# Kernel tuning notes

Hardware: AMD Instinct MI355X
Metric: run time of the kernel (lower is better)

## Reference

```python
import jax, jax.numpy as jnp
import numpy as np

B, C, Q, D = 64, 512, 64, 256  # D = 2 * hidden_size; similarity weight has 3*D = 768 entries


def _length_mask(key, batch, seqlen):
    # realistic padding masks: each row has a random valid prefix length in [seqlen//2, seqlen]
    lens = jax.random.randint(key, (batch,), seqlen // 2, seqlen + 1)
    return (jnp.arange(seqlen)[None, :] < lens[:, None]).astype(jnp.int32)


def setup_inputs() -> dict:
    key = jax.random.key(0)
    k1, k2, k3, k4, k5 = jax.random.split(key, 5)
    context = jax.random.normal(k1, (B, C, D), dtype=jnp.float32)
    question = jax.random.normal(k2, (B, Q, D), dtype=jnp.float32)
    context_mask = _length_mask(k3, B, C)
    question_mask = _length_mask(k4, B, Q)
    w = jax.random.normal(k5, (3 * D,), dtype=jnp.float32) * (1.0 / np.sqrt(3 * D))
    return {"context": context, "question": question,
            "context_mask": context_mask, "question_mask": question_mask, "w": w}


def reference(context, question, context_mask, question_mask, w):
    d = context.shape[-1]
    # Linear([c, q, c*q]) with no bias decomposes exactly into three terms.
    w_c, w_q, w_m = w[:d], w[d:2 * d], w[2 * d:]
    sim = ((context @ w_c)[:, :, None]                      # [B, C, 1]
           + (question @ w_q)[:, None, :]                   # [B, 1, Q]
           + jnp.einsum('bcd,bqd->bcq', context * w_m, question))  # [B, C, Q]
    neg = jnp.finfo(sim.dtype).min
    # context-to-query attention (mask question positions)
    sim_q = jnp.where(question_mask[:, None, :] != 0, sim, neg)
    a = jax.nn.softmax(sim_q, axis=2)                        # [B, C, Q]
    c2q = jnp.einsum('bcq,bqd->bcd', a, question)            # [B, C, D]
    # query-to-context attention (max over Q, mask context positions)
    sim_max = jnp.max(sim, axis=2)                           # [B, C]
    sim_max = jnp.where(context_mask != 0, sim_max, neg)
    b = jax.nn.softmax(sim_max, axis=1)                      # [B, C]
    q2c = jnp.einsum('bc,bcd->bd', b, context)[:, None, :]   # [B, 1, D]
    q2c = jnp.broadcast_to(q2c, context.shape)               # [B, C, D]
    g = jnp.concatenate([context, c2q, context * c2q, context * q2c], axis=-1)
    return g
```

## Files before the change

kernel.cpp:

```cpp
#include <hip/hip_runtime.h>
#include <hip/hip_bf16.h>
#include <float.h>

#define B_ 64
#define C_ 512
#define Q_ 64
#define D_ 256

typedef _Float16 f16x8 __attribute__((ext_vector_type(8)));
typedef float f32x4 __attribute__((ext_vector_type(4)));

union U4H8 { uint4 u; f16x8 h; };
union UH2 { _Float16 h[2]; uint32_t u; };

__device__ __forceinline__ uint32_t packh2(float a, float b) {
  UH2 v; v.h[0] = (_Float16)a; v.h[1] = (_Float16)b; return v.u;
}

__device__ __forceinline__ float wred_sum(float v) {
#pragma unroll
  for (int off = 32; off > 0; off >>= 1) v += __shfl_xor(v, off, 64);
  return v;
}
__device__ __forceinline__ float wred_max(float v) {
#pragma unroll
  for (int off = 32; off > 0; off >>= 1) v = fmaxf(v, __shfl_xor(v, off, 64));
  return v;
}

__global__ __launch_bounds__(256) void k_rowdot(const float* __restrict__ src,
                                                const float* __restrict__ wgt,
                                                float* __restrict__ out, int nrows) {
  int wv = threadIdx.x >> 6, ln = threadIdx.x & 63;
  int row = blockIdx.x * 4 + wv;
  if (row >= nrows) return;
  float4 s4 = *(const float4*)(src + (size_t)row * D_ + 4 * ln);
  float4 w4 = *(const float4*)(wgt + 4 * ln);
  float p = s4.x * w4.x + s4.y * w4.y + s4.z * w4.z + s4.w * w4.w;
  p = wred_sum(p);
  if (ln == 0) out[row] = p;
}

__global__ __launch_bounds__(256) void k_prepack(const float* __restrict__ qst,
                                                 const float* __restrict__ w,
                                                 uint32_t* __restrict__ qraw_img,
                                                 uint32_t* __restrict__ qT_img,
                                                 float* __restrict__ qwq) {
  const int b = blockIdx.x;
  const int sub = blockIdx.y;
  const int t = threadIdx.x;
  const float* qb = qst + (size_t)b * Q_ * D_;
#pragma unroll
  for (int it = 0; it < 8; ++it) {
    int idx = sub * 2048 + it * 256 + t;
    int q = idx >> 7, jp = idx & 127;
    float2 v = *(const float2*)(qb + q * D_ + 2 * jp);
    int ch = jp >> 2;
    int phys = (ch & ~7) | ((ch & 7) ^ (q & 7));
    qraw_img[(size_t)b * 8192 + q * 128 + phys * 4 + (jp & 3)] = packh2(v.x, v.y);
  }
  {
    int d = sub * 64 + (t >> 2);
    uint32_t* dst = qT_img + (size_t)b * 8192 + d * 32;
#pragma unroll
    for (int k = 0; k < 2; ++k) {
      int qc = (t & 3) * 2 + k;
      uint32_t tmp[4];
#pragma unroll
      for (int e = 0; e < 4; ++e) {
        int q0 = qc * 8 + e * 2;
        tmp[e] = packh2(qb[q0 * D_ + d], qb[(q0 + 1) * D_ + d]);
      }
      int pc = qc ^ (d & 7);
      *(uint4*)(dst + pc * 4) = uint4{tmp[0], tmp[1], tmp[2], tmp[3]};
    }
  }
  if (sub == 0) {
    int q = t >> 2, sl = t & 3;
    float p = 0.f;
#pragma unroll
    for (int i = 0; i < 16; ++i) {
      float4 v = *(const float4*)(qb + q * D_ + sl * 64 + i * 4);
      float4 ww = *(const float4*)(w + D_ + sl * 64 + i * 4);
      p += v.x * ww.x + v.y * ww.y + v.z * ww.z + v.w * ww.w;
    }
    p += __shfl_xor(p, 1, 64);
    p += __shfl_xor(p, 2, 64);
    if (sl == 0) qwq[b * Q_ + q] = p;
  }
}

__global__ __launch_bounds__(256, 4) void k_sim(
    const float* __restrict__ ctx, const int* __restrict__ qmask,
    const float* __restrict__ w, const float* __restrict__ qwq_g,
    const uint32_t* __restrict__ qraw_img,
    ushort* __restrict__ P_img, float* __restrict__ simmax_g) {
  __shared__ __align__(16) ushort qraw[Q_ * D_];
  __shared__ float qwq_l[Q_];
  __shared__ int   qml_l[Q_];

  const int bid = blockIdx.x;
  const int b = bid & 63;
  const int c0 = (bid >> 6) * 64;
  const int t = threadIdx.x;
  const int wv = t >> 6, ln = t & 63;
  const int lc = ln & 15;
  const int lg = ln >> 4;
  const int c0w = c0 + wv * 16;

  {
    const uint32_t* qr_src = qraw_img + (size_t)b * 8192;
#pragma unroll
    for (int i = 0; i < 8; ++i)
      __builtin_amdgcn_global_load_lds(
          (const __attribute__((address_space(1))) uint32_t*)(qr_src + i * 1024 + t * 4),
          (__attribute__((address_space(3))) uint32_t*)((uint32_t*)qraw + i * 1024 + t * 4),
          16, 0, 0);
  }

  f16x8 bfrag[8];
  float cwc_p = 0.f;
  const float* crow = ctx + ((size_t)b * C_ + c0w + lc) * D_;
#pragma unroll
  for (int kk = 0; kk < 8; ++kk) {
    int kb = kk * 32 + lg * 8;
    float4 cv0 = *(const float4*)(crow + kb);
    float4 cv1 = *(const float4*)(crow + kb + 4);
    float4 wc0 = *(const float4*)(w + kb);
    float4 wc1 = *(const float4*)(w + kb + 4);
    float4 wm0 = *(const float4*)(w + 2 * D_ + kb);
    float4 wm1 = *(const float4*)(w + 2 * D_ + kb + 4);
    cwc_p += cv0.x * wc0.x + cv0.y * wc0.y + cv0.z * wc0.z + cv0.w * wc0.w
           + cv1.x * wc1.x + cv1.y * wc1.y + cv1.z * wc1.z + cv1.w * wc1.w;
    bfrag[kk][0] = (_Float16)(cv0.x * wm0.x);
    bfrag[kk][1] = (_Float16)(cv0.y * wm0.y);
    bfrag[kk][2] = (_Float16)(cv0.z * wm0.z);
    bfrag[kk][3] = (_Float16)(cv0.w * wm0.w);
    bfrag[kk][4] = (_Float16)(cv1.x * wm1.x);
    bfrag[kk][5] = (_Float16)(cv1.y * wm1.y);
    bfrag[kk][6] = (_Float16)(cv1.z * wm1.z);
    bfrag[kk][7] = (_Float16)(cv1.w * wm1.w);
  }
  float cwc = cwc_p;
  cwc += __shfl_xor(cwc, 16, 64);
  cwc += __shfl_xor(cwc, 32, 64);

  if (t < Q_) { qwq_l[t] = qwq_g[b * Q_ + t]; qml_l[t] = qmask[b * Q_ + t]; }
  __syncthreads();

  f32x4 sacc[4];
#pragma unroll
  for (int tq = 0; tq < 4; ++tq) sacc[tq] = f32x4{0.f, 0.f, 0.f, 0.f};
#pragma unroll
  for (int tq = 0; tq < 4; ++tq) {
    int q = 16 * tq + lc;
#pragma unroll
    for (int kk = 0; kk < 8; ++kk) {
      int ch = lg + 4 * kk;
      int phys = (ch & ~7) | ((ch & 7) ^ (q & 7));
      U4H8 a; a.u = *(const uint4*)((const char*)qraw + q * 512 + phys * 16);
      sacc[tq] = __builtin_amdgcn_mfma_f32_16x16x32_f16(a.h, bfrag[kk], sacc[tq], 0, 0, 0);
    }
  }

  float vals[4][4];
  float rmax = -FLT_MAX;
#pragma unroll
  for (int tq = 0; tq < 4; ++tq) {
    float4 qw4 = *(const float4*)(qwq_l + 16 * tq + 4 * lg);
#pragma unroll
    for (int r = 0; r < 4; ++r) {
      float qv = (r == 0) ? qw4.x : (r == 1) ? qw4.y : (r == 2) ? qw4.z : qw4.w;
      vals[tq][r] = sacc[tq][r] + cwc + qv;
      rmax = fmaxf(rmax, vals[tq][r]);
    }
  }
  rmax = fmaxf(rmax, __shfl_xor(rmax, 16, 64));
  rmax = fmaxf(rmax, __shfl_xor(rmax, 32, 64));
  if (ln < 16) simmax_g[b * C_ + c0w + lc] = rmax;

  float mmax = -FLT_MAX;
#pragma unroll
  for (int tq = 0; tq < 4; ++tq) {
    int4 qm4 = *(const int4*)(qml_l + 16 * tq + 4 * lg);
#pragma unroll
    for (int r = 0; r < 4; ++r) {
      int m = (r == 0) ? qm4.x : (r == 1) ? qm4.y : (r == 2) ? qm4.z : qm4.w;
      vals[tq][r] = m ? vals[tq][r] : -FLT_MAX;
      mmax = fmaxf(mmax, vals[tq][r]);
    }
  }
  mmax = fmaxf(mmax, __shfl_xor(mmax, 16, 64));
  mmax = fmaxf(mmax, __shfl_xor(mmax, 32, 64));
  float esum = 0.f;
#pragma unroll
  for (int tq = 0; tq < 4; ++tq)
#pragma unroll
    for (int r = 0; r < 4; ++r) {
      vals[tq][r] = __expf(vals[tq][r] - mmax);
      esum += vals[tq][r];
    }
  esum += __shfl_xor(esum, 16, 64);
  esum += __shfl_xor(esum, 32, 64);
  float inv = 1.f / esum;
  char* pdst = (char*)(P_img + ((size_t)bid * 4 + wv) * 1024);
#pragma unroll
  for (int tq = 0; tq < 4; ++tq) {
    uint32_t p01 = packh2(vals[tq][0] * inv, vals[tq][1] * inv);
    uint32_t p23 = packh2(vals[tq][2] * inv, vals[tq][3] * inv);
    int qb4 = 16 * tq + 4 * lg;
    *(uint2*)(pdst + lc * 128 + qb4 * 2) = uint2{p01, p23};
  }
}

__global__ __launch_bounds__(256, 4) void k_c2q(
    const float* __restrict__ ctx, const uint32_t* __restrict__ qT_img,
    const ushort* __restrict__ P_img, const float* __restrict__ part,
    float* __restrict__ g) {
  __shared__ __align__(16) ushort qT[D_ * Q_];
  __shared__ float q2c_l[D_];

  const int bid = blockIdx.x;
  const int b = bid & 63;
  const int c0 = (bid >> 6) * 64;
  const int t = threadIdx.x;
  const int wv = t >> 6, ln = t & 63;
  const int lc = ln & 15;
  const int lg = ln >> 4;
  const int c0w = c0 + wv * 16;

  {
    const uint32_t* qt_src = qT_img + (size_t)b * 8192;
#pragma unroll
    for (int i = 0; i < 8; ++i)
      __builtin_amdgcn_global_load_lds(
          (const __attribute__((address_space(1))) uint32_t*)(qt_src + i * 1024 + t * 4),
          (__attribute__((address_space(3))) uint32_t*)((uint32_t*)qT + i * 1024 + t * 4),
          16, 0, 0);
  }
  const char* psrc = (const char*)(P_img + ((size_t)bid * 4 + wv) * 1024);
  U4H8 pf0, pf1;
  pf0.u = *(const uint4*)(psrc + lc * 128 + lg * 16);
  pf1.u = *(const uint4*)(psrc + lc * 128 + lg * 16 + 64);
  {
    float s = 0.f;
#pragma unroll
    for (int k = 0; k < 8; ++k) s += part[((size_t)b * 8 + k) * D_ + t];
    q2c_l[t] = s;
  }
  __syncthreads();

  const float* crow2 = ctx + ((size_t)b * C_ + c0w + lc) * D_;
  float* grow = g + ((size_t)b * C_ + c0w + lc) * (4 * D_);
#pragma unroll 4
  for (int dt = 0; dt < 16; ++dt) {
    f32x4 acc = f32x4{0.f, 0.f, 0.f, 0.f};
    {
      int d = dt * 16 + lc;
      int phys0 = lg ^ (d & 7);
      int phys1 = (lg + 4) ^ (d & 7);
      U4H8 aq0; aq0.u = *(const uint4*)((const char*)qT + d * 128 + phys0 * 16);
      U4H8 aq1; aq1.u = *(const uint4*)((const char*)qT + d * 128 + phys1 * 16);
      acc = __builtin_amdgcn_mfma_f32_16x16x32_f16(aq0.h, pf0.h, acc, 0, 0, 0);
      acc = __builtin_amdgcn_mfma_f32_16x16x32_f16(aq1.h, pf1.h, acc, 0, 0, 0);
    }
    int dcol = dt * 16 + 4 * lg;
    float4 cvv = *(const float4*)(crow2 + dcol);
    float4 q4 = *(const float4*)(q2c_l + dcol);
    *(float4*)(grow + dcol) = cvv;
    float4 c2qv{acc[0], acc[1], acc[2], acc[3]};
    *(float4*)(grow + D_ + dcol) = c2qv;
    float4 p2{cvv.x * c2qv.x, cvv.y * c2qv.y, cvv.z * c2qv.z, cvv.w * c2qv.w};
    *(float4*)(grow + 2 * D_ + dcol) = p2;
    float4 p3{cvv.x * q4.x, cvv.y * q4.y, cvv.z * q4.z, cvv.w * q4.w};
    *(float4*)(grow + 3 * D_ + dcol) = p3;
  }
}

__global__ __launch_bounds__(256) void k_q2c_bs(const float* __restrict__ ctx,
                                                const float* __restrict__ simmax,
                                                const int* __restrict__ cmask,
                                                float* __restrict__ part) {
  int b = blockIdx.x, ch = blockIdx.y, t = threadIdx.x;
  int wv = t >> 6, ln = t & 63;
  __shared__ float bls[C_];
  __shared__ float sred[4];
  __shared__ float ssum[4];
  float v0 = simmax[b * C_ + t], v1 = simmax[b * C_ + 256 + t];
  if (!cmask[b * C_ + t]) v0 = -FLT_MAX;
  if (!cmask[b * C_ + 256 + t]) v1 = -FLT_MAX;
  float mx = wred_max(fmaxf(v0, v1));
  if (ln == 0) sred[wv] = mx;
  __syncthreads();
  float bm = fmaxf(fmaxf(sred[0], sred[1]), fmaxf(sred[2], sred[3]));
  float e0 = __expf(v0 - bm), e1 = __expf(v1 - bm);
  float ps = wred_sum(e0 + e1);
  if (ln == 0) ssum[wv] = ps;
  __syncthreads();
  float bs = ssum[0] + ssum[1] + ssum[2] + ssum[3];
  float invbs = 1.f / bs;
  bls[t] = e0 * invbs;
  bls[256 + t] = e1 * invbs;
  __syncthreads();
  float acc = 0.f;
  int cbeg = ch * 64;
#pragma unroll 4
  for (int c = cbeg; c < cbeg + 64; ++c)
    acc += bls[c] * ctx[((size_t)b * C_ + c) * D_ + t];
  part[((size_t)b * 8 + ch) * D_ + t] = acc;
}

__global__ __launch_bounds__(256, 2) void k_main_fb(
    const float* __restrict__ ctx, const float* __restrict__ qst,
    const int* __restrict__ qmask, const float* __restrict__ w,
    const float* __restrict__ qwq_g, float* __restrict__ g,
    float* __restrict__ simmax_g) {
  __shared__ __align__(16) ushort qraw[Q_ * D_];
  __shared__ __align__(16) ushort qT[D_ * Q_];
  __shared__ __align__(16) ushort pbuf[4][16 * Q_];
  __shared__ float qwq_l[Q_];
  __shared__ int   qml_l[Q_];

  const int bid = blockIdx.x;
  const int b = bid & 63;
  const int c0 = (bid >> 6) * 64;
  const int t = threadIdx.x;
  const int wv = t >> 6, ln = t & 63;
  const int lc = ln & 15;
  const int lg = ln >> 4;
  const int c0w = c0 + wv * 16;
  const float* qb = qst + (size_t)b * Q_ * D_;

  f16x8 bfrag[8];
  float cwc_p = 0.f;
  const float* crow = ctx + ((size_t)b * C_ + c0w + lc) * D_;
  float* grow0 = g + ((size_t)b * C_ + c0w + lc) * (4 * D_);
#pragma unroll
  for (int kk = 0; kk < 8; ++kk) {
    int kb = kk * 32 + lg * 8;
    float4 cv0 = *(const float4*)(crow + kb);
    float4 cv1 = *(const float4*)(crow + kb + 4);
    float4 wc0 = *(const float4*)(w + kb);
    float4 wc1 = *(const float4*)(w + kb + 4);
    float4 wm0 = *(const float4*)(w + 2 * D_ + kb);
    float4 wm1 = *(const float4*)(w + 2 * D_ + kb + 4);
    cwc_p += cv0.x * wc0.x + cv0.y * wc0.y + cv0.z * wc0.z + cv0.w * wc0.w
           + cv1.x * wc1.x + cv1.y * wc1.y + cv1.z * wc1.z + cv1.w * wc1.w;
    bfrag[kk][0] = (_Float16)(cv0.x * wm0.x);
    bfrag[kk][1] = (_Float16)(cv0.y * wm0.y);
    bfrag[kk][2] = (_Float16)(cv0.z * wm0.z);
    bfrag[kk][3] = (_Float16)(cv0.w * wm0.w);
    bfrag[kk][4] = (_Float16)(cv1.x * wm1.x);
    bfrag[kk][5] = (_Float16)(cv1.y * wm1.y);
    bfrag[kk][6] = (_Float16)(cv1.z * wm1.z);
    bfrag[kk][7] = (_Float16)(cv1.w * wm1.w);
    *(float4*)(grow0 + kb) = cv0;
    *(float4*)(grow0 + kb + 4) = cv1;
  }
  float cwc = cwc_p;
  cwc += __shfl_xor(cwc, 16, 64);
  cwc += __shfl_xor(cwc, 32, 64);

#pragma unroll 4
  for (int it = 0; it < 32; ++it) {
    int idx = it * 256 + t;
    int q = idx >> 7, jp = idx & 127;
    float2 v = *(const float2*)(qb + q * D_ + 2 * jp);
    int ch = jp >> 2;
    int phys = (ch & ~7) | ((ch & 7) ^ (q & 7));
    *(uint32_t*)((char*)qraw + q * 512 + phys * 16 + (jp & 3) * 4) = packh2(v.x, v.y);
  }
#pragma unroll 4
  for (int it = 0; it < 32; ++it) {
    int q = t & 63;
    int jp = (t >> 6) + 4 * it;
    float2 v = *(const float2*)(qb + q * D_ + 2 * jp);
    int d0 = 2 * jp, d1 = d0 + 1;
    UH2 h0; h0.h[0] = (_Float16)v.x;
    UH2 h1; h1.h[0] = (_Float16)v.y;
    *(ushort*)((char*)qT + d0 * 128 + (((q >> 3) ^ (d0 & 7)) << 4) + (q & 7) * 2) = (ushort)(h0.u & 0xffff);
    *(ushort*)((char*)qT + d1 * 128 + (((q >> 3) ^ (d1 & 7)) << 4) + (q & 7) * 2) = (ushort)(h1.u & 0xffff);
  }
  if (t < Q_) { qwq_l[t] = qwq_g[b * Q_ + t]; qml_l[t] = qmask[b * Q_ + t]; }
  __syncthreads();

  f32x4 sacc[4];
#pragma unroll
  for (int tq = 0; tq < 4; ++tq) sacc[tq] = f32x4{0.f, 0.f, 0.f, 0.f};
#pragma unroll
  for (int tq = 0; tq < 4; ++tq) {
    int q = 16 * tq + lc;
#pragma unroll
    for (int kk = 0; kk < 8; ++kk) {
      int ch = lg + 4 * kk;
      int phys = (ch & ~7) | ((ch & 7) ^ (q & 7));
      U4H8 a; a.u = *(const uint4*)((const char*)qraw + q * 512 + phys * 16);
      sacc[tq] = __builtin_amdgcn_mfma_f32_16x16x32_f16(a.h, bfrag[kk], sacc[tq], 0, 0, 0);
    }
  }
  float vals[4][4];
  float rmax = -FLT_MAX;
#pragma unroll
  for (int tq = 0; tq < 4; ++tq) {
    float4 qw4 = *(const float4*)(qwq_l + 16 * tq + 4 * lg);
#pragma unroll
    for (int r = 0; r < 4; ++r) {
      float qv = (r == 0) ? qw4.x : (r == 1) ? qw4.y : (r == 2) ? qw4.z : qw4.w;
      vals[tq][r] = sacc[tq][r] + cwc + qv;
      rmax = fmaxf(rmax, vals[tq][r]);
    }
  }
  rmax = fmaxf(rmax, __shfl_xor(rmax, 16, 64));
  rmax = fmaxf(rmax, __shfl_xor(rmax, 32, 64));
  if (ln < 16) simmax_g[b * C_ + c0w + lc] = rmax;
  float mmax = -FLT_MAX;
#pragma unroll
  for (int tq = 0; tq < 4; ++tq) {
    int4 qm4 = *(const int4*)(qml_l + 16 * tq + 4 * lg);
#pragma unroll
    for (int r = 0; r < 4; ++r) {
      int m = (r == 0) ? qm4.x : (r == 1) ? qm4.y : (r == 2) ? qm4.z : qm4.w;
      vals[tq][r] = m ? vals[tq][r] : -FLT_MAX;
      mmax = fmaxf(mmax, vals[tq][r]);
    }
  }
  mmax = fmaxf(mmax, __shfl_xor(mmax, 16, 64));
  mmax = fmaxf(mmax, __shfl_xor(mmax, 32, 64));
  float esum = 0.f;
#pragma unroll
  for (int tq = 0; tq < 4; ++tq)
#pragma unroll
    for (int r = 0; r < 4; ++r) {
      vals[tq][r] = __expf(vals[tq][r] - mmax);
      esum += vals[tq][r];
    }
  esum += __shfl_xor(esum, 16, 64);
  esum += __shfl_xor(esum, 32, 64);
  float inv = 1.f / esum;
#pragma unroll
  for (int tq = 0; tq < 4; ++tq) {
    uint32_t p01 = packh2(vals[tq][0] * inv, vals[tq][1] * inv);
    uint32_t p23 = packh2(vals[tq][2] * inv, vals[tq][3] * inv);
    int qb4 = 16 * tq + 4 * lg;
    int phys = ((qb4 >> 3) ^ (lc & 7));
    char* dst = (char*)pbuf[wv] + lc * 128 + phys * 16 + (qb4 & 7) * 2;
    *(uint2*)dst = uint2{p01, p23};
  }
  f16x8 pfragB[2];
#pragma unroll
  for (int ks = 0; ks < 2; ++ks) {
    int phys = (lg + 4 * ks) ^ (lc & 7);
    U4H8 a; a.u = *(const uint4*)((const char*)pbuf[wv] + lc * 128 + phys * 16);
    pfragB[ks] = a.h;
  }
  const float* crow2 = ctx + ((size_t)b * C_ + c0w + lc) * D_;
  float* grow = g + ((size_t)b * C_ + c0w + lc) * (4 * D_);
#pragma unroll 4
  for (int dt = 0; dt < 16; ++dt) {
    f32x4 acc = f32x4{0.f, 0.f, 0.f, 0.f};
#pragma unroll
    for (int ks = 0; ks < 2; ++ks) {
      int d = dt * 16 + lc;
      int phys = (lg + 4 * ks) ^ (d & 7);
      U4H8 aq; aq.u = *(const uint4*)((const char*)qT + d * 128 + phys * 16);
      acc = __builtin_amdgcn_mfma_f32_16x16x32_f16(aq.h, pfragB[ks], acc, 0, 0, 0);
    }
    int dcol = dt * 16 + 4 * lg;
    float4 cvv = *(const float4*)(crow2 + dcol);
    float4 c2qv{acc[0], acc[1], acc[2], acc[3]};
    *(float4*)(grow + D_ + dcol) = c2qv;
    float4 p2{cvv.x * c2qv.x, cvv.y * c2qv.y, cvv.z * c2qv.z, cvv.w * c2qv.w};
    *(float4*)(grow + 2 * D_ + dcol) = p2;
  }
}

__global__ __launch_bounds__(256) void k_g3q(const float* __restrict__ ctx,
                                             const float* __restrict__ part,
                                             float* __restrict__ g) {
  int b = blockIdx.x, ch = blockIdx.y, t = threadIdx.x;
  __shared__ float q2c_l[D_];
  float s = 0.f;
#pragma unroll
  for (int k = 0; k < 8; ++k) s += part[((size_t)b * 8 + k) * D_ + t];
  q2c_l[t] = s;
  __syncthreads();
  int d4 = t & 63;
  int ro = t >> 6;
  float4 qv = *(const float4*)(q2c_l + 4 * d4);
#pragma unroll 4
  for (int it = 0; it < 16; ++it) {
    int c = ch * 64 + it * 4 + ro;
    float4 cv = *(const float4*)(ctx + ((size_t)b * C_ + c) * D_ + 4 * d4);
    float4 o{cv.x * qv.x, cv.y * qv.y, cv.z * qv.z, cv.w * qv.w};
    *(float4*)(g + ((size_t)b * C_ + c) * (4 * D_) + 3 * D_ + 4 * d4) = o;
  }
}

extern "C" void kernel_launch(void* const* d_in, const int* in_sizes, int n_in,
                              void* d_out, int out_size, void* d_ws, size_t ws_size,
                              hipStream_t stream) {
  const float* ctx   = (const float*)d_in[0];
  const float* qst   = (const float*)d_in[1];
  const int*   cmask = (const int*)d_in[2];
  const int*   qmask = (const int*)d_in[3];
  const float* w     = (const float*)d_in[4];
  float* g  = (float*)d_out;
  float* ws = (float*)d_ws;

  float*    qwq      = ws;
  float*    simmax   = ws + 4096;
  float*    part     = ws + 36864;
  uint32_t* qraw_img = (uint32_t*)(ws + 167936);
  uint32_t* qT_img   = (uint32_t*)(ws + 692224);
  ushort*   P_img    = (ushort*)(ws + 1216512);
  const size_t need_bytes = (size_t)(1216512 + 1048576) * 4;

  if (ws_size >= need_bytes) {
    k_prepack<<<dim3(B_, 4), 256, 0, stream>>>(qst, w, qraw_img, qT_img, qwq);
    k_sim<<<dim3(512), 256, 0, stream>>>(ctx, qmask, w, qwq, qraw_img,
                                         P_img, simmax);
    k_q2c_bs<<<dim3(B_, 8), 256, 0, stream>>>(ctx, simmax, cmask, part);
    k_c2q<<<dim3(512), 256, 0, stream>>>(ctx, qT_img, P_img, part, g);
  } else {
    k_rowdot<<<dim3(B_ * Q_ / 4), 256, 0, stream>>>(qst, w + D_, qwq, B_ * Q_);
    k_main_fb<<<dim3(512), 256, 0, stream>>>(ctx, qst, qmask, w, qwq, g, simmax);
    k_q2c_bs<<<dim3(B_, 8), 256, 0, stream>>>(ctx, simmax, cmask, part);
    k_g3q<<<dim3(B_, 8), 256, 0, stream>>>(ctx, part, g);
  }
}
```

Measured before the change: 60.68 us.

## Fuse query-to-context softmax into k_sim with per-block online partial max/sum

Removes the separate k_q2c_bs launch. Each k_sim block now computes its own masked max over its 64 context rows, the exp-weighted partial sum of context rows, and the partial denominator. k_c2q merges these partials with a log-sum-exp rescale. This saves one kernel launch and a second pass over the context tensor, since ctx rows are re-read while likely still cached. In exchange k_sim gets extra LDS, two block syncs, and more tail work, which may lower occupancy.

```diff
diff --git a/kernel.cpp b/kernel.cpp
--- a/kernel.cpp
+++ b/kernel.cpp
@@ -92,12 +92,16 @@
 
 __global__ __launch_bounds__(256, 4) void k_sim(
     const float* __restrict__ ctx, const int* __restrict__ qmask,
-    const float* __restrict__ w, const float* __restrict__ qwq_g,
-    const uint32_t* __restrict__ qraw_img,
-    ushort* __restrict__ P_img, float* __restrict__ simmax_g) {
+    const int* __restrict__ cmask, const float* __restrict__ w,
+    const float* __restrict__ qwq_g, const uint32_t* __restrict__ qraw_img,
+    ushort* __restrict__ P_img, float* __restrict__ part,
+    float* __restrict__ pmax_g, float* __restrict__ psum_g) {
   __shared__ __align__(16) ushort qraw[Q_ * D_];
   __shared__ float qwq_l[Q_];
   __shared__ int   qml_l[Q_];
+  __shared__ __align__(16) float sred2[64];
+  __shared__ float psum_w[4];
+  __shared__ __align__(16) float pvLDS[4][256];
 
   const int bid = blockIdx.x;
   const int b = bid & 63;
@@ -177,7 +181,6 @@
   }
   rmax = fmaxf(rmax, __shfl_xor(rmax, 16, 64));
   rmax = fmaxf(rmax, __shfl_xor(rmax, 32, 64));
-  if (ln < 16) simmax_g[b * C_ + c0w + lc] = rmax;
 
   float mmax = -FLT_MAX;
 #pragma unroll
@@ -211,11 +214,46 @@
     int qb4 = 16 * tq + 4 * lg;
     *(uint2*)(pdst + lc * 128 + qb4 * 2) = uint2{p01, p23};
   }
+
+  if (ln < 16) {
+    int cm = cmask[b * C_ + c0w + lc];
+    sred2[wv * 16 + lc] = cm ? rmax : -FLT_MAX;
+  }
+  __syncthreads();
+  float M_loc = -FLT_MAX;
+#pragma unroll
+  for (int i = 0; i < 16; ++i) {
+    float4 v4 = *(const float4*)(sred2 + 4 * i);
+    M_loc = fmaxf(M_loc, fmaxf(fmaxf(v4.x, v4.y), fmaxf(v4.z, v4.w)));
+  }
+  float4 pvec{0.f, 0.f, 0.f, 0.f};
+  float ps = 0.f;
+  const float* cbase = ctx + ((size_t)b * C_ + c0w) * D_ + 4 * ln;
+#pragma unroll 4
+  for (int r = 0; r < 16; ++r) {
+    float e = __expf(sred2[wv * 16 + r] - M_loc);
+    ps += e;
+    float4 cv = *(const float4*)(cbase + r * D_);
+    pvec.x += e * cv.x; pvec.y += e * cv.y;
+    pvec.z += e * cv.z; pvec.w += e * cv.w;
+  }
+  *(float4*)(&pvLDS[wv][4 * ln]) = pvec;
+  if (ln == 0) psum_w[wv] = ps;
+  __syncthreads();
+  {
+    float s = pvLDS[0][t] + pvLDS[1][t] + pvLDS[2][t] + pvLDS[3][t];
+    part[((size_t)b * 8 + (bid >> 6)) * D_ + t] = s;
+  }
+  if (t == 0) {
+    pmax_g[b * 8 + (bid >> 6)] = M_loc;
+    psum_g[b * 8 + (bid >> 6)] = psum_w[0] + psum_w[1] + psum_w[2] + psum_w[3];
+  }
 }
 
 __global__ __launch_bounds__(256, 4) void k_c2q(
     const float* __restrict__ ctx, const uint32_t* __restrict__ qT_img,
     const ushort* __restrict__ P_img, const float* __restrict__ part,
+    const float* __restrict__ pmax_g, const float* __restrict__ psum_g,
     float* __restrict__ g) {
   __shared__ __align__(16) ushort qT[D_ * Q_];
   __shared__ float q2c_l[D_];
@@ -243,10 +281,17 @@
   pf0.u = *(const uint4*)(psrc + lc * 128 + lg * 16);
   pf1.u = *(const uint4*)(psrc + lc * 128 + lg * 16 + 64);
   {
-    float s = 0.f;
-#pragma unroll
-    for (int k = 0; k < 8; ++k) s += part[((size_t)b * 8 + k) * D_ + t];
-    q2c_l[t] = s;
+    float M = -FLT_MAX;
+#pragma unroll
+    for (int k = 0; k < 8; ++k) M = fmaxf(M, pmax_g[b * 8 + k]);
+    float den = 0.f, num = 0.f;
+#pragma unroll
+    for (int k = 0; k < 8; ++k) {
+      float sc = __expf(pmax_g[b * 8 + k] - M);
+      den += psum_g[b * 8 + k] * sc;
+      num += part[((size_t)b * 8 + k) * D_ + t] * sc;
+    }
+    q2c_l[t] = num / den;
   }
   __syncthreads();
 
@@ -510,17 +555,19 @@
   float*    qwq      = ws;
   float*    simmax   = ws + 4096;
   float*    part     = ws + 36864;
-  uint32_t* qraw_img = (uint32_t*)(ws + 167936);
-  uint32_t* qT_img   = (uint32_t*)(ws + 692224);
-  ushort*   P_img    = (ushort*)(ws + 1216512);
-  const size_t need_bytes = (size_t)(1216512 + 1048576) * 4;
+  float*    pmax_g   = ws + 167936;
+  float*    psum_g   = ws + 168448;
+  uint32_t* qraw_img = (uint32_t*)(ws + 168960);
+  uint32_t* qT_img   = (uint32_t*)(ws + 693248);
+  ushort*   P_img    = (ushort*)(ws + 1217536);
+  const size_t need_bytes = (size_t)(1217536 + 1048576) * 4;
 
   if (ws_size >= need_bytes) {
     k_prepack<<<dim3(B_, 4), 256, 0, stream>>>(qst, w, qraw_img, qT_img, qwq);
-    k_sim<<<dim3(512), 256, 0, stream>>>(ctx, qmask, w, qwq, qraw_img,
-                                         P_img, simmax);
-    k_q2c_bs<<<dim3(B_, 8), 256, 0, stream>>>(ctx, simmax, cmask, part);
-    k_c2q<<<dim3(512), 256, 0, stream>>>(ctx, qT_img, P_img, part, g);
+    k_sim<<<dim3(512), 256, 0, stream>>>(ctx, qmask, cmask, w, qwq, qraw_img,
+                                         P_img, part, pmax_g, psum_g);
+    k_c2q<<<dim3(512), 256, 0, stream>>>(ctx, qT_img, P_img, part,
+                                         pmax_g, psum_g, g);
   } else {
     k_rowdot<<<dim3(B_ * Q_ / 4), 256, 0, stream>>>(qst, w + D_, qwq, B_ * Q_);
     k_main_fb<<<dim3(512), 256, 0, stream>>>(ctx, qst, qmask, w, qwq, g, simmax);
```

Result: faster. 57.65 us (median of 2 runs) (-5.0%).
